# Kernel optimization log

Hardware: AMD Instinct MI355X
Metric: run time of the kernel (lower is better)

The kernel has to match this reference:

```python
import jax, jax.numpy as jnp
import numpy as np

V, D, H, F, L, B, S = 32000, 1024, 16, 4096, 6, 2, 1024
DH = D // H


def setup_inputs() -> dict:
    key = jax.random.key(0)
    ks = jax.random.split(key, 12)
    n = lambda k, shape: jax.random.normal(k, shape, jnp.float32) * 0.02
    inp = {}
    inp['x'] = jax.random.randint(ks[0], (B, S), 0, V)
    # causal mask: 1 = masked (upper triangle), matches masked_fill(mask==1, -inf)
    inp['mask'] = jnp.triu(jnp.ones((S, S), jnp.int32), k=1)[None, None]
    inp['embed'] = n(ks[1], (V, D))
    inp['wq'] = n(ks[2], (L, D, D)); inp['bq'] = jnp.zeros((L, D), jnp.float32)
    inp['wk'] = n(ks[3], (L, D, D)); inp['bk'] = jnp.zeros((L, D), jnp.float32)
    inp['wv'] = n(ks[4], (L, D, D)); inp['bv'] = jnp.zeros((L, D), jnp.float32)
    inp['wo'] = n(ks[5], (L, D, D)); inp['bo'] = jnp.zeros((L, D), jnp.float32)
    inp['w1'] = n(ks[6], (L, D, F)); inp['b1'] = jnp.zeros((L, F), jnp.float32)
    inp['w2'] = n(ks[7], (L, F, D)); inp['b2'] = jnp.zeros((L, D), jnp.float32)
    inp['ln1_g'] = jnp.ones((L, D), jnp.float32); inp['ln1_b'] = jnp.zeros((L, D), jnp.float32)
    inp['ln2_g'] = jnp.ones((L, D), jnp.float32); inp['ln2_b'] = jnp.zeros((L, D), jnp.float32)
    inp['lnf_g'] = jnp.ones((D,), jnp.float32); inp['lnf_b'] = jnp.zeros((D,), jnp.float32)
    inp['proj_w'] = n(ks[8], (D, V)); inp['proj_b'] = jnp.zeros((V,), jnp.float32)
    return inp


def _layernorm(x, g, b, eps=1e-5):
    mu = jnp.mean(x, axis=-1, keepdims=True)
    var = jnp.var(x, axis=-1, keepdims=True)
    return (x - mu) * jax.lax.rsqrt(var + eps) * g + b


def _positional_encoding(s, d):
    pos = jnp.arange(s, dtype=jnp.float32)[:, None]
    div = jnp.exp(jnp.arange(0, d, 2, dtype=jnp.float32) * (-jnp.log(10000.0) / d))
    pe = jnp.zeros((s, d), jnp.float32)
    pe = pe.at[:, 0::2].set(jnp.sin(pos * div))
    pe = pe.at[:, 1::2].set(jnp.cos(pos * div))
    return pe


def reference(x, mask, embed, wq, bq, wk, bk, wv, bv, wo, bo, w1, b1, w2, b2,
              ln1_g, ln1_b, ln2_g, ln2_b, lnf_g, lnf_b, proj_w, proj_b):
    b_, s_ = x.shape
    h = embed[x] * jnp.sqrt(jnp.float32(D))          # [B,S,D]
    h = h + _positional_encoding(s_, D)[None]
    scale = 1.0 / jnp.sqrt(jnp.float32(DH))

    def layer(h, p):
        Wq, Bq, Wk, Bk, Wv, Bv, Wo, Bo, W1, B1, W2, B2, G1, Be1, G2, Be2 = p
        q = (h @ Wq + Bq).reshape(b_, s_, H, DH).transpose(0, 2, 1, 3)   # [B,H,S,Dh]
        k = (h @ Wk + Bk).reshape(b_, s_, H, DH).transpose(0, 2, 1, 3)
        v = (h @ Wv + Bv).reshape(b_, s_, H, DH).transpose(0, 2, 1, 3)
        scores = jnp.einsum('bhqd,bhkd->bhqk', q, k) * scale            # [B,H,S,S]
        scores = jnp.where(mask == 1, -jnp.inf, scores)
        attn = jax.nn.softmax(scores, axis=-1)
        ctx = jnp.einsum('bhqk,bhkd->bhqd', attn, v)
        ctx = ctx.transpose(0, 2, 1, 3).reshape(b_, s_, D) @ Wo + Bo
        h = _layernorm(h + ctx, G1, Be1)
        ffn = jax.nn.relu(h @ W1 + B1) @ W2 + B2
        h = _layernorm(h + ffn, G2, Be2)
        return h, None

    h, _ = jax.lax.scan(layer, h, (wq, bq, wk, bk, wv, bv, wo, bo,
                                   w1, b1, w2, b2, ln1_g, ln1_b, ln2_g, ln2_b))
    h = _layernorm(h, lnf_g, lnf_b)
    return h @ proj_w + proj_b                                           # [B,S,V]
```

## Files before the change

kernel.cpp:

```cpp
#include <hip/hip_runtime.h>
#include <math.h>

#define D_MODEL 1024
#define NHEADS 16
#define DHEAD 64
#define FDIM 4096
#define NLAYERS 6
#define BATCH 2
#define SEQ 1024
#define NROWS (BATCH*SEQ)
#define VOCAB 32000

typedef __attribute__((ext_vector_type(4))) float f32x4;
typedef __attribute__((ext_vector_type(4))) __bf16 bf16x4;
typedef __attribute__((ext_vector_type(8))) __bf16 bf16x8;

__device__ __forceinline__ void gll16(const void* g, void* l) {
  __builtin_amdgcn_global_load_lds(
      (const __attribute__((address_space(1))) unsigned int*)g,
      (__attribute__((address_space(3))) unsigned int*)l, 16, 0, 0);
}

__global__ __launch_bounds__(256) void transpose_w(
    const float* __restrict__ W, __bf16* __restrict__ Wt, int K, int N) {
  __shared__ __bf16 Ls[64][68];
  const size_t moff = (size_t)blockIdx.z * K * N;
  const float* Wl = W + moff;
  __bf16* Wtl = Wt + moff;
  const int n0 = blockIdx.x * 64, k0 = blockIdx.y * 64;
  const int tid = threadIdx.x;
  #pragma unroll
  for (int p = 0; p < 4; ++p) {
    int e = tid + p * 256;
    int r = e >> 4, c4 = (e & 15) * 4;
    float4 v = *(const float4*)&Wl[(size_t)(k0 + r) * N + n0 + c4];
    Ls[c4 + 0][r] = (__bf16)v.x; Ls[c4 + 1][r] = (__bf16)v.y;
    Ls[c4 + 2][r] = (__bf16)v.z; Ls[c4 + 3][r] = (__bf16)v.w;
  }
  __syncthreads();
  #pragma unroll
  for (int p = 0; p < 4; ++p) {
    int e = tid + p * 256;
    int r2 = e >> 4, c8 = (e & 15) * 4;
    bf16x4 o{Ls[r2][c8], Ls[r2][c8 + 1], Ls[r2][c8 + 2], Ls[r2][c8 + 3]};
    *(bf16x4*)&Wtl[(size_t)(n0 + r2) * K + k0 + c8] = o;
  }
}

struct GemmP {
  const __bf16* A;
  const __bf16* W[3];
  const float* B[3];
  void* C[3];
  int N, K;
};

template<int BM, int RELU, int OUTF32>
__global__ __launch_bounds__(256) void gemm_bf16(GemmP g) {
  constexpr int BK = 64;
  const __bf16* __restrict__ A = g.A;
  const __bf16* __restrict__ W = g.W[blockIdx.z];
  const float* __restrict__ bias = g.B[blockIdx.z];
  const int N = g.N, K = g.K;

  __shared__ __bf16 As[BM * BK];
  __shared__ __bf16 Bs[128 * BK];

  const int tid = threadIdx.x;
  const int lane = tid & 63, w = tid >> 6;
  const int row0 = blockIdx.x * BM, col0 = blockIdx.y * 128;
  const int wm = w >> 1, wn = w & 1;
  const int lr = lane & 15, lk = (lane >> 4) * 8;

  constexpr int MI = BM / 32;
  f32x4 acc[MI][4] = {};

  const __bf16* Ag = A + (size_t)(row0 + w * (BM / 4) + (lane >> 3)) * K + (lane & 7) * 8;
  const __bf16* Wg = W + (size_t)(col0 + w * 32 + (lane >> 3)) * K + (lane & 7) * 8;
  __bf16* Asl = &As[(w * (BM / 4)) * BK];
  __bf16* Bsl = &Bs[(w * 32) * BK];

  for (int k0 = 0; k0 < K; k0 += BK) {
    __syncthreads();
    #pragma unroll
    for (int s = 0; s < BM / 32; ++s)
      gll16(Ag + (size_t)s * 8 * K + k0, Asl + s * 8 * BK);
    #pragma unroll
    for (int s = 0; s < 4; ++s)
      gll16(Wg + (size_t)s * 8 * K + k0, Bsl + s * 8 * BK);
    __syncthreads();

    #pragma unroll
    for (int kk = 0; kk < 2; ++kk) {
      bf16x8 af[MI], bf[4];
      #pragma unroll
      for (int i = 0; i < MI; ++i)
        af[i] = *(const bf16x8*)&As[(wm * (BM / 2) + i * 16 + lr) * BK + kk * 32 + lk];
      #pragma unroll
      for (int j = 0; j < 4; ++j)
        bf[j] = *(const bf16x8*)&Bs[(wn * 64 + j * 16 + lr) * BK + kk * 32 + lk];
      #pragma unroll
      for (int i = 0; i < MI; ++i)
        #pragma unroll
        for (int j = 0; j < 4; ++j)
          acc[i][j] = __builtin_amdgcn_mfma_f32_16x16x32_bf16(af[i], bf[j], acc[i][j], 0, 0, 0);
    }
  }

  #pragma unroll
  for (int i = 0; i < MI; ++i) {
    #pragma unroll
    for (int j = 0; j < 4; ++j) {
      int col = col0 + wn * 64 + j * 16 + lr;
      float bb = bias[col];
      #pragma unroll
      for (int r = 0; r < 4; ++r) {
        int row = row0 + wm * (BM / 2) + i * 16 + (lane >> 4) * 4 + r;
        float v = acc[i][j][r] + bb;
        if (RELU) v = fmaxf(v, 0.0f);
        if (OUTF32) ((float*)g.C[blockIdx.z])[(size_t)row * N + col] = v;
        else ((__bf16*)g.C[blockIdx.z])[(size_t)row * N + col] = (__bf16)v;
      }
    }
  }
}

__global__ __launch_bounds__(256) void attn_kernel(
    const __bf16* __restrict__ Q, const __bf16* __restrict__ K,
    const __bf16* __restrict__ V, __bf16* __restrict__ O) {
  __shared__ __bf16 Ks[64 * 64];
  __shared__ __bf16 Vts[64 * 64];
  __shared__ __bf16 Psm[4][16 * 64];

  const int tid = threadIdx.x;
  const int lane = tid & 63, w = tid >> 6;
  const int q0 = blockIdx.x * 64;
  const int bh = blockIdx.y;
  const int b = bh >> 4, h = bh & 15;
  const size_t base = ((size_t)b * SEQ) * D_MODEL + (size_t)h * DHEAD;

  const int lr = lane & 15;
  const int lk = (lane >> 4) * 8;

  bf16x8 qa[2];
  {
    const __bf16* qp = Q + base + (size_t)(q0 + w * 16 + lr) * D_MODEL;
    qa[0] = *(const bf16x8*)&qp[lk];
    qa[1] = *(const bf16x8*)&qp[32 + lk];
  }

  f32x4 o_acc[4] = {};
  float m[4], l[4];
  #pragma unroll
  for (int r = 0; r < 4; ++r) { m[r] = -1e30f; l[r] = 0.0f; }

  const int nck = q0 / 64 + 1;

  for (int ck = 0; ck < nck; ++ck) {
    const int kv0 = ck * 64;
    __syncthreads();
    #pragma unroll
    for (int c = 0; c < 2; ++c) {
      int e = tid + c * 256;
      int r = e >> 3, d8 = (e & 7) * 8;
      const size_t grow = base + (size_t)(kv0 + r) * D_MODEL + d8;
      bf16x8 kv = *(const bf16x8*)&K[grow];
      *(bf16x8*)&Ks[(r * 64 + d8) ^ ((r & 7) << 3)] = kv;
      bf16x8 vv = *(const bf16x8*)&V[grow];
      #pragma unroll
      for (int j = 0; j < 8; ++j)
        Vts[((d8 + j) * 64 + r) ^ (((d8 + j) & 7) << 3)] = vv[j];
    }
    __syncthreads();

    f32x4 s_acc[4] = {};
    #pragma unroll
    for (int t = 0; t < 4; ++t) {
      int row = t * 16 + lr;
      #pragma unroll
      for (int hh = 0; hh < 2; ++hh) {
        bf16x8 kb = *(const bf16x8*)&Ks[(row * 64 + hh * 32 + lk) ^ ((row & 7) << 3)];
        s_acc[t] = __builtin_amdgcn_mfma_f32_16x16x32_bf16(qa[hh], kb, s_acc[t], 0, 0, 0);
      }
    }

    const bool diag = (ck == nck - 1);
    #pragma unroll
    for (int t = 0; t < 4; ++t) {
      int kvg = kv0 + t * 16 + lr;
      #pragma unroll
      for (int r = 0; r < 4; ++r) {
        float sv = s_acc[t][r] * 0.125f;
        if (diag) {
          int qg = q0 + w * 16 + (lane >> 4) * 4 + r;
          if (kvg > qg) sv = -1e30f;
        }
        s_acc[t][r] = sv;
      }
    }

    #pragma unroll
    for (int r = 0; r < 4; ++r) {
      float cm = fmaxf(fmaxf(s_acc[0][r], s_acc[1][r]), fmaxf(s_acc[2][r], s_acc[3][r]));
      #pragma unroll
      for (int off = 1; off < 16; off <<= 1) cm = fmaxf(cm, __shfl_xor(cm, off, 64));
      float newm = fmaxf(m[r], cm);
      float sc = __expf(m[r] - newm);
      m[r] = newm;
      float psum = 0.0f;
      #pragma unroll
      for (int t = 0; t < 4; ++t) {
        float p = __expf(s_acc[t][r] - newm);
        s_acc[t][r] = p;
        psum += p;
      }
      #pragma unroll
      for (int off = 1; off < 16; off <<= 1) psum += __shfl_xor(psum, off, 64);
      l[r] = l[r] * sc + psum;
      #pragma unroll
      for (int t = 0; t < 4; ++t) o_acc[t][r] *= sc;
    }

    #pragma unroll
    for (int t = 0; t < 4; ++t) {
      #pragma unroll
      for (int r = 0; r < 4; ++r) {
        int ql = (lane >> 4) * 4 + r;
        Psm[w][(ql * 64 + t * 16 + lr) ^ ((ql & 7) << 3)] = (__bf16)(s_acc[t][r]);
      }
    }

    bf16x8 pa[2];
    #pragma unroll
    for (int hh = 0; hh < 2; ++hh)
      pa[hh] = *(const bf16x8*)&Psm[w][(lr * 64 + hh * 32 + lk) ^ ((lr & 7) << 3)];
    #pragma unroll
    for (int t = 0; t < 4; ++t) {
      int row = t * 16 + lr;
      #pragma unroll
      for (int hh = 0; hh < 2; ++hh) {
        bf16x8 vb = *(const bf16x8*)&Vts[(row * 64 + hh * 32 + lk) ^ ((row & 7) << 3)];
        o_acc[t] = __builtin_amdgcn_mfma_f32_16x16x32_bf16(pa[hh], vb, o_acc[t], 0, 0, 0);
      }
    }
  }

  #pragma unroll
  for (int r = 0; r < 4; ++r) {
    float inv = 1.0f / l[r];
    int qg = q0 + w * 16 + (lane >> 4) * 4 + r;
    #pragma unroll
    for (int t = 0; t < 4; ++t)
      O[base + (size_t)qg * D_MODEL + t * 16 + lr] = (__bf16)(o_acc[t][r] * inv);
  }
}

template<int HASRES>
__global__ __launch_bounds__(256) void addln_kernel(
    const __bf16* __restrict__ X, const __bf16* __restrict__ Rr,
    const float* __restrict__ g, const float* __restrict__ bb,
    __bf16* __restrict__ Out) {
  const int row = blockIdx.x;
  const int tid = threadIdx.x;
  const size_t rb = (size_t)row * D_MODEL + tid * 4;
  bf16x4 xv = *(const bf16x4*)&X[rb];
  float v[4];
  float s = 0.0f, ss = 0.0f;
  if (HASRES) {
    bf16x4 rv = *(const bf16x4*)&Rr[rb];
    #pragma unroll
    for (int i = 0; i < 4; ++i) {
      v[i] = (float)xv[i] + (float)rv[i];
      s += v[i]; ss += v[i] * v[i];
    }
  } else {
    #pragma unroll
    for (int i = 0; i < 4; ++i) { v[i] = (float)xv[i]; s += v[i]; ss += v[i] * v[i]; }
  }
  #pragma unroll
  for (int off = 32; off; off >>= 1) { s += __shfl_xor(s, off, 64); ss += __shfl_xor(ss, off, 64); }
  __shared__ float red[8];
  const int lane = tid & 63, w = tid >> 6;
  if (lane == 0) { red[w] = s; red[4 + w] = ss; }
  __syncthreads();
  s = red[0] + red[1] + red[2] + red[3];
  ss = red[4] + red[5] + red[6] + red[7];
  float mean = s * (1.0f / D_MODEL);
  float var = ss * (1.0f / D_MODEL) - mean * mean;
  float rs = rsqrtf(var + 1e-5f);
  const int d0 = tid * 4;
  bf16x4 ov;
  #pragma unroll
  for (int i = 0; i < 4; ++i)
    ov[i] = (__bf16)((v[i] - mean) * rs * g[d0 + i] + bb[d0 + i]);
  *(bf16x4*)&Out[rb] = ov;
}

__global__ __launch_bounds__(256) void embed_kernel(
    const int* __restrict__ x, const float* __restrict__ embed,
    __bf16* __restrict__ H) {
  const int row = blockIdx.x;
  const int spos = row & (SEQ - 1);
  const int tok = x[row];
  const int tid = threadIdx.x;
  const int d0 = tid * 4;
  float4 e4 = *(const float4*)&embed[(size_t)tok * D_MODEL + d0];
  float ev[4] = {e4.x, e4.y, e4.z, e4.w};
  bf16x4 ov;
  #pragma unroll
  for (int i = 0; i < 4; ++i) {
    int d = d0 + i;
    float div = expf((float)(2 * (d >> 1)) * (-9.2103403719761836f / (float)D_MODEL));
    float ang = (float)spos * div;
    float pe = (d & 1) ? cosf(ang) : sinf(ang);
    ov[i] = (__bf16)(ev[i] * 32.0f + pe);
  }
  *(bf16x4*)&H[(size_t)row * D_MODEL + d0] = ov;
}

extern "C" void kernel_launch(void* const* d_in, const int* in_sizes, int n_in,
                              void* d_out, int out_size, void* d_ws, size_t ws_size,
                              hipStream_t stream) {
  const int* x = (const int*)d_in[0];
  const float* embed = (const float*)d_in[2];
  const float* wq = (const float*)d_in[3];
  const float* bq = (const float*)d_in[4];
  const float* wk = (const float*)d_in[5];
  const float* bk = (const float*)d_in[6];
  const float* wv = (const float*)d_in[7];
  const float* bv = (const float*)d_in[8];
  const float* wo = (const float*)d_in[9];
  const float* bo = (const float*)d_in[10];
  const float* w1 = (const float*)d_in[11];
  const float* b1 = (const float*)d_in[12];
  const float* w2 = (const float*)d_in[13];
  const float* b2 = (const float*)d_in[14];
  const float* ln1g = (const float*)d_in[15];
  const float* ln1b = (const float*)d_in[16];
  const float* ln2g = (const float*)d_in[17];
  const float* ln2b = (const float*)d_in[18];
  const float* lnfg = (const float*)d_in[19];
  const float* lnfb = (const float*)d_in[20];
  const float* pw = (const float*)d_in[21];
  const float* pb = (const float*)d_in[22];
  float* out = (float*)d_out;

  char* wsp = (char*)d_ws;
  size_t off = 0;
  auto alloc = [&](size_t bytes) {
    void* p = wsp + off; off = (off + bytes + 255) & ~(size_t)255; return p;
  };
  const size_t RD2 = (size_t)NROWS * D_MODEL * 2;
  __bf16* Xb   = (__bf16*)alloc(RD2);
  __bf16* Qb   = (__bf16*)alloc(RD2);
  __bf16* Kb   = (__bf16*)alloc(RD2);
  __bf16* Vb   = (__bf16*)alloc(RD2);
  __bf16* CTXb = (__bf16*)alloc(RD2);
  __bf16* Tb   = (__bf16*)alloc(RD2);
  __bf16* H1b  = (__bf16*)alloc(RD2);
  __bf16* FFb  = Qb;
  const size_t DD = (size_t)D_MODEL * D_MODEL;
  const size_t DF = (size_t)D_MODEL * FDIM;
  __bf16* wqt = (__bf16*)alloc(NLAYERS * DD * 2);
  __bf16* wkt = (__bf16*)alloc(NLAYERS * DD * 2);
  __bf16* wvt = (__bf16*)alloc(NLAYERS * DD * 2);
  __bf16* wot = (__bf16*)alloc(NLAYERS * DD * 2);
  __bf16* w1t = (__bf16*)alloc(NLAYERS * DF * 2);
  __bf16* w2t = (__bf16*)alloc(NLAYERS * DF * 2);
  __bf16* pwt = (__bf16*)alloc((size_t)D_MODEL * VOCAB * 2);

  transpose_w<<<dim3(16, 16, NLAYERS), 256, 0, stream>>>(wq, wqt, D_MODEL, D_MODEL);
  transpose_w<<<dim3(16, 16, NLAYERS), 256, 0, stream>>>(wk, wkt, D_MODEL, D_MODEL);
  transpose_w<<<dim3(16, 16, NLAYERS), 256, 0, stream>>>(wv, wvt, D_MODEL, D_MODEL);
  transpose_w<<<dim3(16, 16, NLAYERS), 256, 0, stream>>>(wo, wot, D_MODEL, D_MODEL);
  transpose_w<<<dim3(64, 16, NLAYERS), 256, 0, stream>>>(w1, w1t, D_MODEL, FDIM);
  transpose_w<<<dim3(16, 64, NLAYERS), 256, 0, stream>>>(w2, w2t, FDIM, D_MODEL);
  transpose_w<<<dim3(500, 16, 1), 256, 0, stream>>>(pw, pwt, D_MODEL, VOCAB);

  embed_kernel<<<NROWS, 256, 0, stream>>>(x, embed, Xb);

  for (int l = 0; l < NLAYERS; ++l) {
    GemmP g{};
    g.A = Xb; g.N = D_MODEL; g.K = D_MODEL;
    g.W[0] = wqt + l * DD; g.W[1] = wkt + l * DD; g.W[2] = wvt + l * DD;
    g.B[0] = bq + l * D_MODEL; g.B[1] = bk + l * D_MODEL; g.B[2] = bv + l * D_MODEL;
    g.C[0] = Qb; g.C[1] = Kb; g.C[2] = Vb;
    gemm_bf16<128, 0, 0><<<dim3(NROWS / 128, D_MODEL / 128, 3), 256, 0, stream>>>(g);

    attn_kernel<<<dim3(SEQ / 64, BATCH * NHEADS), 256, 0, stream>>>(Qb, Kb, Vb, CTXb);

    GemmP go{};
    go.A = CTXb; go.N = D_MODEL; go.K = D_MODEL;
    go.W[0] = wot + l * DD; go.B[0] = bo + l * D_MODEL; go.C[0] = Tb;
    gemm_bf16<64, 0, 0><<<dim3(NROWS / 64, D_MODEL / 128, 1), 256, 0, stream>>>(go);

    addln_kernel<1><<<NROWS, 256, 0, stream>>>(Xb, Tb, ln1g + l * D_MODEL, ln1b + l * D_MODEL, H1b);

    GemmP g1{};
    g1.A = H1b; g1.N = FDIM; g1.K = D_MODEL;
    g1.W[0] = w1t + l * DF; g1.B[0] = b1 + l * FDIM; g1.C[0] = FFb;
    gemm_bf16<128, 1, 0><<<dim3(NROWS / 128, FDIM / 128, 1), 256, 0, stream>>>(g1);

    GemmP g2{};
    g2.A = FFb; g2.N = D_MODEL; g2.K = FDIM;
    g2.W[0] = w2t + l * DF; g2.B[0] = b2 + l * D_MODEL; g2.C[0] = Tb;
    gemm_bf16<64, 0, 0><<<dim3(NROWS / 64, D_MODEL / 128, 1), 256, 0, stream>>>(g2);

    addln_kernel<1><<<NROWS, 256, 0, stream>>>(H1b, Tb, ln2g + l * D_MODEL, ln2b + l * D_MODEL, Xb);
  }

  addln_kernel<0><<<NROWS, 256, 0, stream>>>(Xb, nullptr, lnfg, lnfb, H1b);

  GemmP gp{};
  gp.A = H1b; gp.N = VOCAB; gp.K = D_MODEL;
  gp.W[0] = pwt; gp.B[0] = pb; gp.C[0] = out;
  gemm_bf16<128, 0, 1><<<dim3(NROWS / 128, VOCAB / 128, 1), 256, 0, stream>>>(gp);
}
```

Baseline: 1.680 ms.

## Double-buffer GEMM LDS tiles with XOR swizzle and XCD-aware block remap

The bf16 GEMM now keeps two LDS buffers and issues the global-to-LDS loads for the next K tile before computing on the current one, so memory latency overlaps the MFMA work. The k-chunk index of each loaded row is XOR-swizzled by the row index, and the fragment reads apply the same swizzle, to avoid LDS bank conflicts. Block ids are remapped so that consecutive tiles land on the same XCD, which should improve L2 reuse. Doubling LDS can lower occupancy. The remap assumes the block count divides evenly by 8, and the prefetch relies on global_load_lds completing before the barrier at the end of the loop.

```diff
diff --git a/kernel.cpp b/kernel.cpp
--- a/kernel.cpp
+++ b/kernel.cpp
@@ -63,48 +63,66 @@
   const float* __restrict__ bias = g.B[blockIdx.z];
   const int N = g.N, K = g.K;
 
-  __shared__ __bf16 As[BM * BK];
-  __shared__ __bf16 Bs[128 * BK];
+  __shared__ __bf16 As[2][BM * BK];
+  __shared__ __bf16 Bs[2][128 * BK];
 
   const int tid = threadIdx.x;
   const int lane = tid & 63, w = tid >> 6;
-  const int row0 = blockIdx.x * BM, col0 = blockIdx.y * 128;
+
+  const int gx = gridDim.x;
+  const int nblk = gx * gridDim.y;
+  const int id = blockIdx.x + blockIdx.y * gx;
+  const int per = nblk >> 3;
+  const int sid = (id & 7) * per + (id >> 3);
+  const int row0 = (sid % gx) * BM;
+  const int col0 = (sid / gx) * 128;
+
   const int wm = w >> 1, wn = w & 1;
-  const int lr = lane & 15, lk = (lane >> 4) * 8;
+  const int lr = lane & 15, rsw = lr & 7;
 
   constexpr int MI = BM / 32;
   f32x4 acc[MI][4] = {};
 
-  const __bf16* Ag = A + (size_t)(row0 + w * (BM / 4) + (lane >> 3)) * K + (lane & 7) * 8;
-  const __bf16* Wg = W + (size_t)(col0 + w * 32 + (lane >> 3)) * K + (lane & 7) * 8;
-  __bf16* Asl = &As[(w * (BM / 4)) * BK];
-  __bf16* Bsl = &Bs[(w * 32) * BK];
-
-  for (int k0 = 0; k0 < K; k0 += BK) {
-    __syncthreads();
+  const int swg = ((lane & 7) ^ (lane >> 3)) * 8;
+  const __bf16* Ag = A + (size_t)(row0 + w * (BM / 4) + (lane >> 3)) * K + swg;
+  const __bf16* Wg = W + (size_t)(col0 + w * 32 + (lane >> 3)) * K + swg;
+
+  const int NT = K / BK;
+
+  auto stage = [&](int buf, int t) {
+    const int k0 = t * BK;
     #pragma unroll
     for (int s = 0; s < BM / 32; ++s)
-      gll16(Ag + (size_t)s * 8 * K + k0, Asl + s * 8 * BK);
+      gll16(Ag + (size_t)s * 8 * K + k0, &As[buf][(w * (BM / 4) + s * 8) * BK]);
     #pragma unroll
     for (int s = 0; s < 4; ++s)
-      gll16(Wg + (size_t)s * 8 * K + k0, Bsl + s * 8 * BK);
-    __syncthreads();
-
+      gll16(Wg + (size_t)s * 8 * K + k0, &Bs[buf][(w * 32 + s * 8) * BK]);
+  };
+
+  stage(0, 0);
+  __syncthreads();
+
+  int cur = 0;
+  for (int t = 0; t < NT; ++t) {
+    if (t + 1 < NT) stage(cur ^ 1, t + 1);
     #pragma unroll
     for (int kk = 0; kk < 2; ++kk) {
+      const int gsw = ((kk * 4 + (lane >> 4)) ^ rsw) * 8;
       bf16x8 af[MI], bf[4];
       #pragma unroll
       for (int i = 0; i < MI; ++i)
-        af[i] = *(const bf16x8*)&As[(wm * (BM / 2) + i * 16 + lr) * BK + kk * 32 + lk];
+        af[i] = *(const bf16x8*)&As[cur][(wm * (BM / 2) + i * 16 + lr) * BK + gsw];
       #pragma unroll
       for (int j = 0; j < 4; ++j)
-        bf[j] = *(const bf16x8*)&Bs[(wn * 64 + j * 16 + lr) * BK + kk * 32 + lk];
+        bf[j] = *(const bf16x8*)&Bs[cur][(wn * 64 + j * 16 + lr) * BK + gsw];
       #pragma unroll
       for (int i = 0; i < MI; ++i)
         #pragma unroll
         for (int j = 0; j < 4; ++j)
           acc[i][j] = __builtin_amdgcn_mfma_f32_16x16x32_bf16(af[i], bf[j], acc[i][j], 0, 0, 0);
     }
+    __syncthreads();
+    cur ^= 1;
   }
 
   #pragma unroll
```

Result: faster. 1.585 ms (-5.6%).
